# Performance work log

Hardware: AMD Instinct MI355X
Metric: run time of the kernel (lower is better)

## Reference

```python
import jax, jax.numpy as jnp
import numpy as np
from jax import lax

D_MODEL, D_INNER, D_STATE, D_CONV, DT_RANK = 1024, 2048, 16, 4, 64
B_SZ, L = 2, 2048


def silu(v):
    return v * jax.nn.sigmoid(v)


def setup_inputs() -> dict:
    key = jax.random.key(0)
    ks = jax.random.split(key, 9)
    s = 0.02
    x = jax.random.normal(ks[0], (B_SZ, L, D_MODEL), jnp.float32)
    W_in = jax.random.normal(ks[1], (D_MODEL, 2 * D_INNER), jnp.float32) * s
    conv_w = jax.random.normal(ks[2], (D_INNER, D_CONV), jnp.float32) * 0.1  # depthwise kernel
    conv_b = jax.random.normal(ks[3], (D_INNER,), jnp.float32) * 0.01
    W_xproj = jax.random.normal(ks[4], (D_INNER, DT_RANK + 2 * D_STATE), jnp.float32) * s
    W_dt = jax.random.normal(ks[5], (DT_RANK, D_INNER), jnp.float32) * s
    b_dt = jax.random.normal(ks[6], (D_INNER,), jnp.float32) * 0.01
    A_log = jnp.log(jnp.tile(jnp.arange(1, D_STATE + 1, dtype=jnp.float32), (D_INNER, 1)))
    D = jnp.ones((D_INNER,), jnp.float32)
    W_out = jax.random.normal(ks[7], (D_INNER, D_MODEL), jnp.float32) * s
    return dict(x=x, W_in=W_in, conv_w=conv_w, conv_b=conv_b, W_xproj=W_xproj,
                W_dt=W_dt, b_dt=b_dt, A_log=A_log, D=D, W_out=W_out)


def reference(x, W_in, conv_w, conv_b, W_xproj, W_dt, b_dt, A_log, D, W_out):
    # in_proj, split into conv path u and gate res
    xr = x @ W_in                                  # (B, L, 2*d_inner)
    u, res = jnp.split(xr, 2, axis=-1)
    # causal depthwise conv1d (left-pad d_conv-1), then SiLU
    uc = jnp.swapaxes(u, 1, 2)                     # (B, C, L)
    uc = lax.conv_general_dilated(
        uc, conv_w[:, None, :], window_strides=(1,),
        padding=[(D_CONV - 1, 0)], feature_group_count=D_INNER,
        dimension_numbers=('NCH', 'OIH', 'NCH'))
    uc = uc + conv_b[None, :, None]
    u = silu(jnp.swapaxes(uc, 1, 2))               # (B, L, d_inner)
    # S6 projections
    x_dbl = u @ W_xproj                            # (B, L, dt_rank + 2*N)
    dt_low = x_dbl[..., :DT_RANK]
    Bm = x_dbl[..., DT_RANK:DT_RANK + D_STATE]     # (B, L, N)
    Cm = x_dbl[..., DT_RANK + D_STATE:]            # (B, L, N)
    dt = jax.nn.softplus(dt_low @ W_dt + b_dt)     # (B, L, d_inner)
    A = -jnp.exp(A_log)                            # (d_inner, N)
    # selective scan over time
    def step(h, inp):
        dt_t, B_t, C_t, u_t = inp                  # (B,d), (B,N), (B,N), (B,d)
        dA = jnp.exp(dt_t[:, :, None] * A)         # (B, d, N)
        dBu = dt_t[:, :, None] * B_t[:, None, :] * u_t[:, :, None]
        h = dA * h + dBu
        y = jnp.sum(h * C_t[:, None, :], axis=-1)  # (B, d)
        return h, y
    h0 = jnp.zeros((B_SZ, D_INNER, D_STATE), u.dtype)
    xs = (jnp.swapaxes(dt, 0, 1), jnp.swapaxes(Bm, 0, 1),
          jnp.swapaxes(Cm, 0, 1), jnp.swapaxes(u, 0, 1))
    _, ys = lax.scan(step, h0, xs)
    y = jnp.swapaxes(ys, 0, 1) + u * D             # (B, L, d_inner)
    # gate and out_proj
    y = y * silu(res)
    return y @ W_out
```

## Files before the change

### kernel.cpp

```cpp
#include <hip/hip_runtime.h>
#include <cstdint>
#include <cstddef>

#define DMODEL 1024
#define DINNER 2048
#define DSTATE 16
#define DCONV  4
#define DTRANK 64
#define BSZ    2
#define SEQL   2048
#define MROWS  (BSZ*SEQL)
#define NCHUNK 32
#define CLEN   (SEQL/NCHUNK)

typedef __bf16 bf16;
typedef bf16  bf16x8 __attribute__((ext_vector_type(8)));
typedef bf16  bf16x4 __attribute__((ext_vector_type(4)));
typedef float floatx4 __attribute__((ext_vector_type(4)));

#define EPILDC 136
#define SLDC   64

__device__ __forceinline__ float fsigmoid(float x){ return 1.f/(1.f+__expf(-x)); }
__device__ __forceinline__ float fsilu(float x){ return x*fsigmoid(x); }

__device__ __forceinline__ void gload_lds16(const void* g, void* l){
  __builtin_amdgcn_global_load_lds((__attribute__((address_space(1))) void*)g,
                                   (__attribute__((address_space(3))) void*)l,
                                   16, 0, 0);
}

__global__ void k_prep(const float* __restrict__ x, bf16* __restrict__ xb,
                       const float* __restrict__ W_in, const float* __restrict__ W_out,
                       const float* __restrict__ W_xproj, const float* __restrict__ W_dt,
                       bf16* __restrict__ WinT, bf16* __restrict__ WoutT,
                       bf16* __restrict__ WxT, bf16* __restrict__ WdtT){
  __shared__ float tile[32][33];
  int b = blockIdx.x;
  if (b < 4096){
    int i = (b*256 + threadIdx.x)*4;
    float4 v = *(const float4*)(x + i);
    bf16x4 o; o[0]=(bf16)v.x; o[1]=(bf16)v.y; o[2]=(bf16)v.z; o[3]=(bf16)v.w;
    *(bf16x4*)(xb + i) = o;
    return;
  }
  b -= 4096;
  const float* in; bf16* out; int R, C, outR, nbx;
  if      (b < 4096)            { in=W_in;    out=WinT;  R=1024; C=4096; outR=4096; nbx=128; }
  else if (b < 4096+2048)       { b-=4096;    in=W_out;  out=WoutT; R=2048; C=1024; outR=1024; nbx=32; }
  else if (b < 4096+2048+256)   { b-=6144;    in=W_xproj;out=WxT;  R=2048; C=96;   outR=128;  nbx=4; }
  else                          { b-=6400;    in=W_dt;   out=WdtT; R=64;   C=2048; outR=2048; nbx=64; }
  int c0 = (b % nbx)*32, r0 = (b / nbx)*32;
  int tx = threadIdx.x & 31, ty = threadIdx.x >> 5;
  #pragma unroll
  for (int ii=0; ii<4; ++ii){
    int r = r0 + ty + ii*8, c = c0 + tx;
    float v = 0.f;
    if (r < R && c < C) v = in[(size_t)r*C + c];
    tile[ty+ii*8][tx] = v;
  }
  __syncthreads();
  #pragma unroll
  for (int ii=0; ii<4; ++ii){
    int orow = c0 + ty + ii*8;
    int ocol = r0 + tx;
    if (orow < outR && ocol < R) out[(size_t)orow*R + ocol] = (bf16)tile[tx][ty+ii*8];
  }
}

template<int EPI>
__global__ __launch_bounds__(256)
void k_gemm_bt(const bf16* __restrict__ A, const bf16* __restrict__ Bt,
               int M, int N, int K,
               float* __restrict__ C0, bf16* __restrict__ C1, bf16* __restrict__ C2,
               const float* __restrict__ bias){
  __shared__ bf16 lds[17408];
  const int tid  = threadIdx.x;
  const int lane = tid & 63;
  const int wave = tid >> 6;
  const int quad = lane >> 4;
  const int mrow = lane & 15;
  const int wr = wave >> 1, wc = wave & 1;
  const int bm = blockIdx.y * 128, bn = blockIdx.x * 128;
  const int Ks   = K / gridDim.z;
  const int kbeg = blockIdx.z * Ks;

  floatx4 acc[4][4];
  #pragma unroll
  for (int i=0;i<4;++i)
    #pragma unroll
    for (int j=0;j<4;++j) acc[i][j] = (floatx4){0.f,0.f,0.f,0.f};

  const int ar0 = tid >> 2;
  const int kc  = ((tid & 3) ^ ((ar0 >> 1) & 3)) * 8;
  const bf16* Ag0 = A  + (size_t)(bm + ar0)      * K + kc;
  const bf16* Ag1 = A  + (size_t)(bm + ar0 + 64) * K + kc;
  const bf16* Bg0 = Bt + (size_t)(bn + ar0)      * K + kc;
  const bf16* Bg1 = Bt + (size_t)(bn + ar0 + 64) * K + kc;
  const int ksl = (mrow >> 1) & 3;

  auto stage = [&](int k0, int p){
    bf16* bA = lds + p*4096;
    bf16* bB = lds + 8192 + p*4096;
    gload_lds16(Ag0 + k0, bA + (size_t)tid*8);
    gload_lds16(Ag1 + k0, bA + (size_t)(256+tid)*8);
    gload_lds16(Bg0 + k0, bB + (size_t)tid*8);
    gload_lds16(Bg1 + k0, bB + (size_t)(256+tid)*8);
  };

  stage(kbeg, 0);
  int p = 0;
  for (int k0 = kbeg; k0 < kbeg + Ks; k0 += 32){
    __syncthreads();
    if (k0 + 32 < kbeg + Ks) stage(k0 + 32, p ^ 1);
    const bf16* bA = lds + p*4096;
    const bf16* bB = lds + 8192 + p*4096;
    bf16x8 af[4], bfr[4];
    #pragma unroll
    for (int i=0;i<4;++i)
      af[i] = *(const bf16x8*)(bA + (wr*64 + i*16 + mrow)*32 + (quad ^ ksl)*8);
    #pragma unroll
    for (int j=0;j<4;++j)
      bfr[j] = *(const bf16x8*)(bB + (wc*64 + j*16 + mrow)*32 + (quad ^ ksl)*8);
    #pragma unroll
    for (int i=0;i<4;++i)
      #pragma unroll
      for (int j=0;j<4;++j)
        acc[i][j] = __builtin_amdgcn_mfma_f32_16x16x32_bf16(af[i], bfr[j], acc[i][j], 0,0,0);
    p ^= 1;
  }

  if (EPI == 0){
    float* Cz = C0 + (size_t)blockIdx.z * M * N;
    #pragma unroll
    for (int i=0;i<4;++i){
      #pragma unroll
      for (int r=0;r<4;++r){
        int row = bm + wr*64 + i*16 + quad*4 + r;
        #pragma unroll
        for (int j=0;j<4;++j){
          int col = bn + wc*64 + j*16 + mrow;
          Cz[(size_t)row*N + col] = acc[i][j][r];
        }
      }
    }
  } else {
    __syncthreads();
    const bool isres = (bn >= DINNER);
    #pragma unroll
    for (int i=0;i<4;++i)
      #pragma unroll
      for (int r=0;r<4;++r){
        int lrow = wr*64 + i*16 + quad*4 + r;
        #pragma unroll
        for (int j=0;j<4;++j){
          int lcol = wc*64 + j*16 + mrow;
          float v = acc[i][j][r];
          lds[lrow*EPILDC + lcol] = (bf16)(isres ? fsilu(v) : v);
        }
      }
    __syncthreads();
    bf16* dst = isres ? (C2 + (bn - DINNER)) : (C1 + bn);
    const int rr = tid >> 1, hh = (tid & 1)*64;
    #pragma unroll
    for (int i=0;i<8;++i)
      *(bf16x8*)(dst + (size_t)(bm + rr)*DINNER + hh + i*8) =
        *(const bf16x8*)(lds + rr*EPILDC + hh + i*8);
  }
}

__global__ void k_xdbl_reduce(const float* __restrict__ part, float* __restrict__ xdbl,
                              bf16* __restrict__ dtlowb){
  int t = blockIdx.x*blockDim.x + threadIdx.x;
  int i4 = t*4;
  floatx4 acc = (floatx4){0.f,0.f,0.f,0.f};
  #pragma unroll
  for (int z=0; z<8; ++z)
    acc += *(const floatx4*)(part + (size_t)z*MROWS*128 + i4);
  *(floatx4*)(xdbl + i4) = acc;
  int r = i4 >> 7, c = i4 & 127;
  if (c < DTRANK){
    bf16x4 o; o[0]=(bf16)acc[0]; o[1]=(bf16)acc[1]; o[2]=(bf16)acc[2]; o[3]=(bf16)acc[3];
    *(bf16x4*)(dtlowb + (size_t)r*DTRANK + c) = o;
  }
}

__global__ void k_out_reduce(const float* __restrict__ part, float* __restrict__ out){
  int i4 = (blockIdx.x*blockDim.x + threadIdx.x)*4;
  floatx4 a = *(const floatx4*)(part + i4);
  floatx4 b = *(const floatx4*)(part + (size_t)MROWS*DMODEL + i4);
  *(floatx4*)(out + i4) = a + b;
}

__global__ void k_conv_silu(const bf16* __restrict__ u_pre,
                            const float* __restrict__ conv_w,
                            const float* __restrict__ conv_b,
                            bf16* __restrict__ ub){
  int t   = blockIdx.x*blockDim.x + threadIdx.x;
  int d4  = (t & (DINNER/4-1))*4;
  int row = t >> 9;
  int l   = row & (SEQL-1);
  float4 cb = *(const float4*)(conv_b + d4);
  float acc[4] = {cb.x, cb.y, cb.z, cb.w};
  float4 w0 = *(const float4*)(conv_w + (d4+0)*4);
  float4 w1 = *(const float4*)(conv_w + (d4+1)*4);
  float4 w2 = *(const float4*)(conv_w + (d4+2)*4);
  float4 w3 = *(const float4*)(conv_w + (d4+3)*4);
  float wk[4][4] = {{w0.x,w0.y,w0.z,w0.w},{w1.x,w1.y,w1.z,w1.w},
                    {w2.x,w2.y,w2.z,w2.w},{w3.x,w3.y,w3.z,w3.w}};
  #pragma unroll
  for (int k=0;k<4;++k){
    int lk = l + k - 3;
    if (lk >= 0){
      bf16x4 uv = *(const bf16x4*)(u_pre + (size_t)(row + k - 3)*DINNER + d4);
      #pragma unroll
      for (int j=0;j<4;++j) acc[j] += (float)uv[j] * wk[j][k];
    }
  }
  bf16x4 o;
  #pragma unroll
  for (int j=0;j<4;++j) o[j] = (bf16)fsilu(acc[j]);
  *(bf16x4*)(ub + (size_t)row*DINNER + d4) = o;
}

__device__ __forceinline__ void dt_tile_stage(const bf16* __restrict__ dtlow,
                                              const bf16* __restrict__ WdtT,
                                              int base_row, int d0, int tid,
                                              bf16* sdt, bf16* swdt){
  int r  = tid >> 2;
  int c2 = (tid & 3)*2, sw = r & 7;
  const bf16* gA = dtlow + (size_t)(base_row + r)*DTRANK + c2*8;
  const bf16* gB = WdtT  + (size_t)(d0 + r)*DTRANK + c2*8;
  *(bf16x8*)(sdt  + r*64 + ((c2  )^sw)*8) = *(const bf16x8*)(gA);
  *(bf16x8*)(sdt  + r*64 + ((c2+1)^sw)*8) = *(const bf16x8*)(gA + 8);
  *(bf16x8*)(swdt + r*64 + ((c2  )^sw)*8) = *(const bf16x8*)(gB);
  *(bf16x8*)(swdt + r*64 + ((c2+1)^sw)*8) = *(const bf16x8*)(gB + 8);
}

__device__ __forceinline__ void dt_tile_compute(const float* __restrict__ b_dt,
                                                int d0, int tid,
                                                bf16* sdt, const bf16* swdt){
  int wave = tid >> 6, lane = tid & 63;
  int quad = lane >> 4, mrow = lane & 15;
  int arow = wave*16 + mrow;
  bf16x8 af0 = *(const bf16x8*)(sdt + arow*64 + ((quad    ) ^ (arow&7))*8);
  bf16x8 af1 = *(const bf16x8*)(sdt + arow*64 + ((quad + 4) ^ (arow&7))*8);
  #pragma unroll
  for (int dj=0; dj<4; ++dj){
    int brow = dj*16 + mrow;
    bf16x8 bf0 = *(const bf16x8*)(swdt + brow*64 + ((quad    ) ^ (brow&7))*8);
    bf16x8 bf1 = *(const bf16x8*)(swdt + brow*64 + ((quad + 4) ^ (brow&7))*8);
    floatx4 a = (floatx4){0.f,0.f,0.f,0.f};
    a = __builtin_amdgcn_mfma_f32_16x16x32_bf16(af0, bf0, a, 0,0,0);
    a = __builtin_amdgcn_mfma_f32_16x16x32_bf16(af1, bf1, a, 0,0,0);
    float bias = b_dt[d0 + dj*16 + mrow];
    #pragma unroll
    for (int rr=0; rr<4; ++rr){
      float z = a[rr] + bias;
      float sp = fmaxf(z, 0.f) + __logf(1.f + __expf(-fabsf(z)));
      sdt[(wave*16 + quad*4 + rr)*64 + dj*16 + mrow] = (bf16)sp;
    }
  }
}

__global__ void k_scan_phase1(const bf16* __restrict__ dtlow, const bf16* __restrict__ WdtT,
                              const float* __restrict__ b_dt,
                              const bf16* __restrict__ ub,
                              const float* __restrict__ x_dbl, const float* __restrict__ A_log,
                              float* __restrict__ Pbuf, float* __restrict__ Sbuf){
  __shared__ bf16 sdt[64*64], sub[64*SLDC], swdt[64*64];
  __shared__ float sB[64*16];
  const int tid = threadIdx.x;
  int t  = blockIdx.x*256 + tid;
  int g  = t & 3;
  int d  = (t >> 2) & (DINNER-1);
  int dloc = d & 63, d0 = d & ~63;
  int bc = t >> 13;
  int c  = bc & (NCHUNK-1);
  int b  = bc >> 5;
  int base_row = b*SEQL + c*CLEN;
  {
    int r = tid >> 2, ch = (tid & 3)*16;
    const bf16* gu = ub + (size_t)(base_row + r)*DINNER + d0 + ch;
    *(bf16x8*)(sub + r*SLDC + ch)     = *(const bf16x8*)(gu);
    *(bf16x8*)(sub + r*SLDC + ch + 8) = *(const bf16x8*)(gu + 8);
    int q = tid & 3;
    *(floatx4*)(sB + r*16 + q*4) =
      *(const floatx4*)(x_dbl + (size_t)(base_row + r)*128 + DTRANK + q*4);
    dt_tile_stage(dtlow, WdtT, base_row, d0, tid, sdt, swdt);
  }
  floatx4 alog = *(const floatx4*)(A_log + d*DSTATE + g*4);
  float an[4];
  #pragma unroll
  for (int n=0;n<4;++n) an[n] = -__expf(alog[n]);
  __syncthreads();
  dt_tile_compute(b_dt, d0, tid, sdt, swdt);
  __syncthreads();
  float sumdt = 0.f, S[4] = {0.f,0.f,0.f,0.f};
  #pragma unroll 8
  for (int s=0; s<CLEN; ++s){
    float dtv = (float)sdt[s*SLDC + dloc];
    float du  = dtv * (float)sub[s*SLDC + dloc];
    floatx4 Bv = *(const floatx4*)(sB + s*16 + g*4);
    sumdt += dtv;
    #pragma unroll
    for (int n=0;n<4;++n){
      float e = __expf(dtv*an[n]);
      S[n]  = fmaf(S[n], e, du*Bv[n]);
    }
  }
  size_t ob = ((size_t)bc*DINNER + d)*DSTATE + g*4;
  floatx4 Pv, Sv = {S[0],S[1],S[2],S[3]};
  #pragma unroll
  for (int n=0;n<4;++n) Pv[n] = __expf(an[n]*sumdt);
  *(floatx4*)(Pbuf + ob) = Pv;
  *(floatx4*)(Sbuf + ob) = Sv;
}

__global__ void k_scan_phase2(const float* __restrict__ Pbuf, float* __restrict__ Sbuf){
  int t = blockIdx.x*blockDim.x + threadIdx.x;
  int b   = t >> 15;
  int rem = t & 32767;
  float h = 0.f;
  for (int c=0;c<NCHUNK;++c){
    size_t ix = (size_t)(b*NCHUNK + c)*DINNER*DSTATE + rem;
    float p = Pbuf[ix], s = Sbuf[ix];
    Sbuf[ix] = h;
    h = fmaf(p, h, s);
  }
}

__global__ void k_scan_phase3(const bf16* __restrict__ dtlow, const bf16* __restrict__ WdtT,
                              const float* __restrict__ b_dt,
                              const bf16* __restrict__ ub,
                              const float* __restrict__ x_dbl, const float* __restrict__ A_log,
                              const float* __restrict__ Dvec, const float* __restrict__ Hin,
                              const bf16* __restrict__ resb, bf16* __restrict__ yb){
  __shared__ bf16 sdt[64*64], sub[64*SLDC], srs[64*SLDC], swdt[64*64];
  __shared__ float sBC[64*32];
  bf16* syb = swdt;
  const int tid = threadIdx.x;
  int t  = blockIdx.x*256 + tid;
  int g  = t & 3;
  int d  = (t >> 2) & (DINNER-1);
  int dloc = d & 63, d0 = d & ~63;
  int bc = t >> 13;
  int c  = bc & (NCHUNK-1);
  int b  = bc >> 5;
  int base_row = b*SEQL + c*CLEN;
  {
    int r = tid >> 2, ch = (tid & 3)*16;
    const bf16* gu = ub   + (size_t)(base_row + r)*DINNER + d0 + ch;
    const bf16* gr = resb + (size_t)(base_row + r)*DINNER + d0 + ch;
    *(bf16x8*)(sub + r*SLDC + ch)     = *(const bf16x8*)(gu);
    *(bf16x8*)(sub + r*SLDC + ch + 8) = *(const bf16x8*)(gu + 8);
    *(bf16x8*)(srs + r*SLDC + ch)     = *(const bf16x8*)(gr);
    *(bf16x8*)(srs + r*SLDC + ch + 8) = *(const bf16x8*)(gr + 8);
    int q = tid & 3;
    const float* gx = x_dbl + (size_t)(base_row + r)*128 + DTRANK;
    *(floatx4*)(sBC + r*32 + q*4)      = *(const floatx4*)(gx + q*4);
    *(floatx4*)(sBC + r*32 + 16 + q*4) = *(const floatx4*)(gx + DSTATE + q*4);
    dt_tile_stage(dtlow, WdtT, base_row, d0, tid, sdt, swdt);
  }
  floatx4 alog = *(const floatx4*)(A_log + d*DSTATE + g*4);
  float an[4];
  #pragma unroll
  for (int n=0;n<4;++n) an[n] = -__expf(alog[n]);
  floatx4 h = *(const floatx4*)(Hin + ((size_t)bc*DINNER + d)*DSTATE + g*4);
  float Dd = Dvec[d];
  __syncthreads();
  dt_tile_compute(b_dt, d0, tid, sdt, swdt);
  __syncthreads();
  #pragma unroll 8
  for (int s=0; s<CLEN; ++s){
    float dtv = (float)sdt[s*SLDC + dloc];
    float uv  = (float)sub[s*SLDC + dloc];
    float du  = dtv*uv;
    floatx4 Bv = *(const floatx4*)(sBC + s*32 + g*4);
    floatx4 Cv = *(const floatx4*)(sBC + s*32 + 16 + g*4);
    float y = 0.f;
    #pragma unroll
    for (int n=0;n<4;++n){
      float e = __expf(dtv*an[n]);
      h[n] = fmaf(h[n], e, du*Bv[n]);
      y = fmaf(h[n], Cv[n], y);
    }
    y += __shfl_xor(y, 1);
    y += __shfl_xor(y, 2);
    if (g == 0){
      y = (y + uv*Dd) * (float)srs[s*SLDC + dloc];
      syb[s*64 + dloc] = (bf16)y;
    }
  }
  __syncthreads();
  {
    int r = tid >> 2, ch = (tid & 3)*16;
    bf16* gy = yb + (size_t)(base_row + r)*DINNER + d0 + ch;
    *(bf16x8*)(gy)     = *(const bf16x8*)(syb + r*64 + ch);
    *(bf16x8*)(gy + 8) = *(const bf16x8*)(syb + r*64 + ch + 8);
  }
}

extern "C" void kernel_launch(void* const* d_in, const int* in_sizes, int n_in,
                              void* d_out, int out_size, void* d_ws, size_t ws_size,
                              hipStream_t stream){
  const float* x      = (const float*)d_in[0];
  const float* W_in   = (const float*)d_in[1];
  const float* conv_w = (const float*)d_in[2];
  const float* conv_b = (const float*)d_in[3];
  const float* W_xproj= (const float*)d_in[4];
  const float* W_dt   = (const float*)d_in[5];
  const float* b_dt   = (const float*)d_in[6];
  const float* A_log  = (const float*)d_in[7];
  const float* Dv     = (const float*)d_in[8];
  const float* W_out  = (const float*)d_in[9];
  float* out = (float*)d_out;

  uint8_t* wp = (uint8_t*)d_ws;
  auto alloc = [&](size_t bytes)->void*{ void* p = wp; wp += (bytes + 255) & ~(size_t)255; return p; };
  bf16*  xb     = (bf16*) alloc((size_t)MROWS*DMODEL*2);
  bf16*  WinT   = (bf16*) alloc((size_t)2*DINNER*DMODEL*2);
  bf16*  WoutT  = (bf16*) alloc((size_t)DMODEL*DINNER*2);
  bf16*  WxT    = (bf16*) alloc((size_t)128*DINNER*2);
  bf16*  WdtT   = (bf16*) alloc((size_t)DINNER*DTRANK*2);
  bf16*  updt   = (bf16*) alloc((size_t)MROWS*DINNER*2);
  float* scanPS = (float*)alloc((size_t)2*BSZ*NCHUNK*DSTATE*DINNER*4);
  float* Pbuf   = scanPS;
  float* Sbuf   = scanPS + (size_t)BSZ*NCHUNK*DSTATE*DINNER;
  float* xdbl_part = scanPS;
  float* outpart   = (float*)updt;
  bf16*  resb   = (bf16*) alloc((size_t)MROWS*DINNER*2);
  bf16*  ub     = (bf16*) alloc((size_t)MROWS*DINNER*2);
  float* xdbl   = (float*)alloc((size_t)MROWS*128*4);
  bf16*  dtlowb = (bf16*) alloc((size_t)MROWS*DTRANK*2);
  bf16*  yb     = (bf16*) alloc((size_t)MROWS*DINNER*2);

  k_prep<<<4096 + 4096+2048+256+128, 256, 0, stream>>>(x, xb, W_in, W_out, W_xproj, W_dt,
                                                       WinT, WoutT, WxT, WdtT);

  k_gemm_bt<1><<<dim3(4096/128, 4096/128), 256, 0, stream>>>(xb, WinT, MROWS, 2*DINNER, DMODEL, nullptr, updt, resb, nullptr);
  k_conv_silu<<<MROWS*DINNER/4/256, 256, 0, stream>>>(updt, conv_w, conv_b, ub);
  k_gemm_bt<0><<<dim3(1, 4096/128, 8), 256, 0, stream>>>(ub, WxT, MROWS, 128, DINNER, xdbl_part, nullptr, nullptr, nullptr);
  k_xdbl_reduce<<<(MROWS*128/4)/256, 256, 0, stream>>>(xdbl_part, xdbl, dtlowb);
  k_scan_phase1<<<BSZ*NCHUNK*DINNER*4/256, 256, 0, stream>>>(dtlowb, WdtT, b_dt, ub, xdbl, A_log, Pbuf, Sbuf);
  k_scan_phase2<<<BSZ*DINNER*DSTATE/256, 256, 0, stream>>>(Pbuf, Sbuf);
  k_scan_phase3<<<BSZ*NCHUNK*DINNER*4/256, 256, 0, stream>>>(dtlowb, WdtT, b_dt, ub, xdbl, A_log, Dv, Sbuf, resb, yb);
  k_gemm_bt<0><<<dim3(1024/128, 4096/128, 2), 256, 0, stream>>>(yb, WoutT, MROWS, DMODEL, DINNER, outpart, nullptr, nullptr, nullptr);
  k_out_reduce<<<(MROWS*DMODEL/4)/256, 256, 0, stream>>>(outpart, out);
}
```

Baseline: 312.4 us.

## Add 256x256-tile double-buffered in_proj GEMM with direct-to-LDS loads

Replaces the 128x128-tile in_proj GEMM with a dedicated 256x256-tile, 512-thread kernel. It uses 128KB of dynamic LDS, XOR-swizzled direct global-to-LDS loads, double buffering with split-stage prefetch, and setprio around the MFMA bursts. The larger tile raises arithmetic intensity and overlaps loads with compute. In exchange the grid shrinks to 256 blocks, and the big LDS footprint limits occupancy to one block per CU, which is under-filled on a 256-CU part.

```diff
diff --git a/kernel.cpp b/kernel.cpp
--- a/kernel.cpp
+++ b/kernel.cpp
@@ -65,6 +65,111 @@
     int orow = c0 + ty + ii*8;
     int ocol = r0 + tx;
     if (orow < outR && ocol < R) out[(size_t)orow*R + ocol] = (bf16)tile[tx][ty+ii*8];
+  }
+}
+
+__global__ __launch_bounds__(512, 2)
+void k_gemm_in256(const bf16* __restrict__ A, const bf16* __restrict__ Bt,
+                  bf16* __restrict__ C1, bf16* __restrict__ C2){
+  extern __shared__ __align__(16) bf16 lds[];
+  const int tid  = threadIdx.x;
+  const int lane = tid & 63;
+  const int wave = tid >> 6;
+  const int quad = lane >> 4;
+  const int mrow = lane & 15;
+  const int wr = wave >> 2, wc = wave & 3;
+  const int bm = blockIdx.y * 256, bn = blockIdx.x * 256;
+
+  floatx4 acc[8][4];
+  #pragma unroll
+  for (int i=0;i<8;++i)
+    #pragma unroll
+    for (int j=0;j<4;++j) acc[i][j] = (floatx4){0.f,0.f,0.f,0.f};
+
+  auto stage_unit = [&](int kt, int p, int mat, int h){
+    const bf16* G = mat ? Bt : A;
+    const int gb  = mat ? bn : bm;
+    bf16* dst = lds + (mat ? 32768 : 0) + p*16384 + h*8192 + tid*8;
+    #pragma unroll
+    for (int l=0; l<2; ++l){
+      int L  = l*512 + tid;
+      int rl = (L >> 3) + h*128;
+      int cg = (L & 7) ^ (rl & 7);
+      gload_lds16(G + (size_t)(gb + rl)*1024 + kt*64 + cg*8, dst + l*4096);
+    }
+  };
+
+  stage_unit(0,0,0,0); stage_unit(0,0,1,0); stage_unit(0,0,0,1); stage_unit(0,0,1,1);
+
+  for (int kt = 0; kt < 16; ++kt){
+    const int p = kt & 1;
+    const bf16* bA = lds + p*16384;
+    const bf16* bB = lds + 32768 + p*16384;
+    #pragma unroll
+    for (int q=0; q<4; ++q){
+      const int mh = q & 1, kk = q >> 1;
+      if (q == 0){
+        if (kt < 15){
+          stage_unit(kt+1, p^1, 0, 0); stage_unit(kt+1, p^1, 1, 0);
+          asm volatile("s_waitcnt vmcnt(4)" ::: "memory");
+        } else {
+          asm volatile("s_waitcnt vmcnt(0)" ::: "memory");
+        }
+      }
+      if (q == 1 && kt < 15){
+        stage_unit(kt+1, p^1, 0, 1); stage_unit(kt+1, p^1, 1, 1);
+      }
+      asm volatile("s_barrier" ::: "memory");
+      bf16x8 af[4], bfr[4];
+      #pragma unroll
+      for (int i=0;i<4;++i){
+        int r = wr*128 + mh*64 + i*16 + mrow;
+        af[i] = *(const bf16x8*)(bA + r*64 + ((((kk<<2)|quad) ^ (r&7))*8));
+      }
+      #pragma unroll
+      for (int j=0;j<4;++j){
+        int r = wc*64 + j*16 + mrow;
+        bfr[j] = *(const bf16x8*)(bB + r*64 + ((((kk<<2)|quad) ^ (r&7))*8));
+      }
+      __builtin_amdgcn_s_setprio(1);
+      #pragma unroll
+      for (int i=0;i<4;++i)
+        #pragma unroll
+        for (int j=0;j<4;++j)
+          acc[mh*4+i][j] = __builtin_amdgcn_mfma_f32_16x16x32_bf16(af[i], bfr[j], acc[mh*4+i][j], 0,0,0);
+      __builtin_amdgcn_s_setprio(0);
+      asm volatile("s_barrier" ::: "memory");
+    }
+  }
+
+  const bool isres = (bn >= DINNER);
+  bf16* dst0 = isres ? (C2 + (bn - DINNER)) : (C1 + bn);
+  #pragma unroll
+  for (int h=0; h<2; ++h){
+    asm volatile("s_barrier" ::: "memory");
+    if (wr == h){
+      #pragma unroll
+      for (int a=0;a<8;++a){
+        #pragma unroll
+        for (int r=0;r<4;++r){
+          int lrow = (a>>2)*64 + (a&3)*16 + quad*4 + r;
+          #pragma unroll
+          for (int j=0;j<4;++j){
+            int lcol = wc*64 + j*16 + mrow;
+            float v = acc[a][j][r];
+            lds[lrow*264 + lcol] = (bf16)(isres ? fsilu(v) : v);
+          }
+        }
+      }
+    }
+    asm volatile("s_barrier" ::: "memory");
+    {
+      int rr = tid >> 2, seg = (tid & 3)*64;
+      bf16* gy = dst0 + (size_t)(bm + h*128 + rr)*DINNER + seg;
+      #pragma unroll
+      for (int i=0;i<8;++i)
+        *(bf16x8*)(gy + i*8) = *(const bf16x8*)(lds + rr*264 + seg + i*8);
+    }
   }
 }
 
@@ -435,10 +540,17 @@
   bf16*  dtlowb = (bf16*) alloc((size_t)MROWS*DTRANK*2);
   bf16*  yb     = (bf16*) alloc((size_t)MROWS*DINNER*2);
 
+  static bool lds_attr_set = false;
+  if (!lds_attr_set){
+    hipFuncSetAttribute((const void*)k_gemm_in256,
+                        hipFuncAttributeMaxDynamicSharedMemorySize, 131072);
+    lds_attr_set = true;
+  }
+
   k_prep<<<4096 + 4096+2048+256+128, 256, 0, stream>>>(x, xb, W_in, W_out, W_xproj, W_dt,
                                                        WinT, WoutT, WxT, WdtT);
 
-  k_gemm_bt<1><<<dim3(4096/128, 4096/128), 256, 0, stream>>>(xb, WinT, MROWS, 2*DINNER, DMODEL, nullptr, updt, resb, nullptr);
+  k_gemm_in256<<<dim3(4096/256, 4096/256), 512, 131072, stream>>>(xb, WinT, updt, resb);
   k_conv_silu<<<MROWS*DINNER/4/256, 256, 0, stream>>>(updt, conv_w, conv_b, ub);
   k_gemm_bt<0><<<dim3(1, 4096/128, 8), 256, 0, stream>>>(ub, WxT, MROWS, 128, DINNER, xdbl_part, nullptr, nullptr, nullptr);
   k_xdbl_reduce<<<(MROWS*128/4)/256, 256, 0, stream>>>(xdbl_part, xdbl, dtlowb);
```

Result: no change. 311.9 us (-0.1%).
